# Optimization experiments

Hardware: AMD Instinct MI355X
Metric: run time of the kernel (lower is better)

## Reference

```python
import math
import jax, jax.numpy as jnp
import numpy as np

B, S, D = 4, 2048, 1024
H, HD = 16, 64
NUM_BUCKETS = 32
MAX_DISTANCE = 128
EPS = 1e-6
ENC_S = 512


def _relative_position_bucket(relative_position):
    # bidirectional=False path
    num_buckets = NUM_BUCKETS
    rp = -jnp.minimum(relative_position, 0)  # [S, S] nonneg
    max_exact = num_buckets // 2
    is_small = rp < max_exact
    scale = (num_buckets - max_exact) / math.log(MAX_DISTANCE / max_exact)
    large = max_exact + (jnp.log(jnp.maximum(rp, 1).astype(jnp.float32) / max_exact) * scale).astype(jnp.int32)
    large = jnp.minimum(large, num_buckets - 1)
    return jnp.where(is_small, rp, large)


def compute_bias(rel_emb, q_len, k_len):
    ctx = jnp.arange(q_len)[:, None]
    mem = jnp.arange(k_len)[None, :]
    bucket = _relative_position_bucket(mem - ctx)          # [q, k] int
    values = rel_emb[bucket]                                # [q, k, H]
    return jnp.transpose(values, (2, 0, 1))[None]           # [1, H, q, k]


def setup_inputs() -> dict:
    key = jax.random.key(0)
    ks = jax.random.split(key, 8)
    std = 0.02
    return {
        "input_ids": jax.random.normal(ks[0], (B, S, D), jnp.float32),
        "encoder_output": jax.random.normal(ks[1], (B, ENC_S, D), jnp.float32),
        "wq": jax.random.normal(ks[2], (D, H * HD), jnp.float32) * std,
        "wk": jax.random.normal(ks[3], (D, H * HD), jnp.float32) * std,
        "wv": jax.random.normal(ks[4], (D, H * HD), jnp.float32) * std,
        "wo": jax.random.normal(ks[5], (H * HD, D), jnp.float32) * std,
        "rel_emb": jax.random.normal(ks[6], (NUM_BUCKETS, H), jnp.float32) * std,
        "ln_w": jnp.ones((D,), jnp.float32),
    }


def reference(input_ids, encoder_output, wq, wk, wv, wo, rel_emb, ln_w):
    origin = input_ids
    # MT5LayerNorm: RMS norm, no mean subtraction, no bias
    variance = jnp.mean(jnp.square(input_ids.astype(jnp.float32)), axis=-1, keepdims=True)
    x = (input_ids * jax.lax.rsqrt(variance + EPS)) * ln_w

    q = (x @ wq).reshape(B, S, H, HD)
    k = (x @ wk).reshape(B, S, H, HD)
    v = (x @ wv).reshape(B, S, H, HD)

    # NOTE: T5-style attention has no 1/sqrt(d) scaling
    scores = jnp.einsum("bqhd,bkhd->bhqk", q, k)
    scores = scores + compute_bias(rel_emb, S, S)
    attn = jax.nn.softmax(scores, axis=-1)
    ctx = jnp.einsum("bhqk,bkhd->bqhd", attn, v).reshape(B, S, H * HD)
    attn_out = ctx @ wo

    # residual connection (dropout is identity at rate 0 / eval)
    return origin + attn_out
```

## Files before the change

### kernel.cpp

```cpp
#include <hip/hip_runtime.h>
#include <hip/hip_bf16.h>
#include <math.h>

#define S_LEN 2048
#define D_DIM 1024
#define NHEAD 16

typedef __attribute__((ext_vector_type(8))) short bf16x8;
typedef __attribute__((ext_vector_type(4))) float floatx4;

__device__ __forceinline__ short f32_bf16(float f) {
  union { float f; unsigned u; } v; v.f = f;
  unsigned r = v.u + 0x7FFFu + ((v.u >> 16) & 1u);
  return (short)(r >> 16);
}

__device__ __forceinline__ float exp2_fast(float x) {
#if __has_builtin(__builtin_amdgcn_exp2f)
  return __builtin_amdgcn_exp2f(x);
#else
  float r; asm("v_exp_f32 %0, %1" : "=v"(r) : "v"(x)); return r;
#endif
}

__device__ __forceinline__ void gload16(const void* g, void* l) {
  __builtin_amdgcn_global_load_lds((const __attribute__((address_space(1))) unsigned*)g,
                                   (__attribute__((address_space(3))) unsigned*)l,
                                   16, 0, 0);
}

__global__ __launch_bounds__(256) void prep_k(const float* __restrict__ x,
                                              const float* __restrict__ lnw,
                                              const float* __restrict__ wq,
                                              const float* __restrict__ wk,
                                              const float* __restrict__ wv,
                                              const float* __restrict__ wo,
                                              short* __restrict__ xb,
                                              short* __restrict__ oqkv,
                                              short* __restrict__ owo) {
  if (blockIdx.x < 8192) {
    int row = blockIdx.x;
    const float4* xr = (const float4*)(x + (size_t)row * D_DIM);
    float4 v = xr[threadIdx.x];
    float ss = v.x*v.x + v.y*v.y + v.z*v.z + v.w*v.w;
    #pragma unroll
    for (int off = 32; off > 0; off >>= 1) ss += __shfl_xor(ss, off);
    __shared__ float red[4];
    if ((threadIdx.x & 63) == 0) red[threadIdx.x >> 6] = ss;
    __syncthreads();
    float scale = rsqrtf((red[0]+red[1]+red[2]+red[3]) * (1.f/D_DIM) + 1e-6f);
    float4 wv4 = ((const float4*)lnw)[threadIdx.x];
    short4 o;
    o.x = f32_bf16(v.x*scale*wv4.x);
    o.y = f32_bf16(v.y*scale*wv4.y);
    o.z = f32_bf16(v.z*scale*wv4.z);
    o.w = f32_bf16(v.w*scale*wv4.w);
    ((short4*)xb)[(size_t)row*256 + threadIdx.x] = o;
  } else {
    __shared__ float tile[64][65];
    int id = blockIdx.x - 8192;
    int m  = id >> 8;
    int tt = id & 255;
    int tn = tt >> 4, tk = tt & 15;
    const float* src = (m == 0) ? wq : (m == 1) ? wk : (m == 2) ? wv : wo;
    float scale = (m == 0) ? 1.44269504f : 1.0f;
    int t = threadIdx.x;
    int kl  = t >> 4;
    int nl4 = t & 15;
    #pragma unroll
    for (int i = 0; i < 4; i++) {
      int k = i*16 + kl;
      float4 v = *(const float4*)&src[(size_t)(tk*64 + k)*1024 + tn*64 + nl4*4];
      tile[k][nl4*4+0] = v.x;
      tile[k][nl4*4+1] = v.y;
      tile[k][nl4*4+2] = v.z;
      tile[k][nl4*4+3] = v.w;
    }
    __syncthreads();
    short* dst = (m < 3) ? oqkv : owo;
    size_t nbase = (m < 3) ? (size_t)m * 1024 : 0;
    #pragma unroll
    for (int i = 0; i < 2; i++) {
      int idx = i*256 + t;
      int nl = idx >> 3;
      int g  = idx & 7;
      short tmp[8];
      #pragma unroll
      for (int j = 0; j < 8; j++) tmp[j] = f32_bf16(tile[g*8 + j][nl] * scale);
      *(bf16x8*)&dst[(nbase + tn*64 + nl)*1024 + tk*64 + g*8] = *(bf16x8*)tmp;
    }
  }
}

template<bool WRITE_VT, bool ADD_RES>
__global__ __launch_bounds__(512) void gemm256(const short* __restrict__ A,
                                               const short* __restrict__ Bt,
                                               short* __restrict__ Cb,
                                               float* __restrict__ Cf,
                                               const float* __restrict__ res,
                                               short* __restrict__ vt,
                                               int N, int NBN) {
  __shared__ __align__(16) short As[4][256*32];
  __shared__ __align__(16) short Bs[4][128*32];
  const int tid = threadIdx.x;
  const int w = tid >> 6, lane = tid & 63, quad = lane >> 4, l16 = lane & 15;
  const int wm = w >> 2, wn = w & 3;
  const int id = blockIdx.x;
  const int o = (id & 7) * (gridDim.x >> 3) + (id >> 3);
  const int bm = o / NBN, bn = o % NBN;
  const short* Ag = A  + (size_t)bm * 256 * 1024;
  const short* Bg = Bt + (size_t)bn * 128 * 1024;
  const int r4 = lane >> 2, c4 = lane & 3;
  const int lc  = c4 ^ ((r4 >> 1) & 3);
  const int swz = (quad ^ ((l16 >> 1) & 3)) * 8;

  floatx4 acc[8][2] = {};

  #define SA(t_) do {                                                          \
    gload16(Ag + (size_t)((w    )*16 + r4) * 1024 + (t_)*32 + lc*8,            \
            &As[(t_) & 3][(w    )*512]);                                       \
    gload16(Ag + (size_t)((w + 8)*16 + r4) * 1024 + (t_)*32 + lc*8,            \
            &As[(t_) & 3][(w + 8)*512]);                                       \
  } while (0)
  #define SB(t_) do {                                                          \
    gload16(Bg + (size_t)((w    )*16 + r4) * 1024 + (t_)*32 + lc*8,            \
            &Bs[(t_) & 3][(w    )*512]);                                       \
  } while (0)

  #define PH(t_, STG_, VMW_) do {                                              \
    const short* Ab = &As[(t_) & 3][0];                                        \
    const short* Bb = &Bs[(t_) & 3][0];                                        \
    bf16x8 af[8], bf0, bf1;                                                    \
    _Pragma("unroll")                                                          \
    for (int i = 0; i < 8; i++)                                                \
      af[i] = *(const bf16x8*)&Ab[(wm*128 + i*16 + l16)*32 + swz];             \
    bf0 = *(const bf16x8*)&Bb[(wn*32 +  0 + l16)*32 + swz];                    \
    if (STG_) SA((t_) + 3);                                                    \
    asm volatile("s_waitcnt lgkmcnt(0)");                                      \
    __builtin_amdgcn_sched_barrier(0);                                         \
    __builtin_amdgcn_s_setprio(1);                                             \
    _Pragma("unroll")                                                          \
    for (int i = 0; i < 8; i++)                                                \
      acc[i][0] = __builtin_amdgcn_mfma_f32_16x16x32_bf16(af[i], bf0, acc[i][0], 0, 0, 0); \
    __builtin_amdgcn_s_setprio(0);                                             \
    bf1 = *(const bf16x8*)&Bb[(wn*32 + 16 + l16)*32 + swz];                    \
    if (STG_) SB((t_) + 3);                                                    \
    asm volatile("s_waitcnt lgkmcnt(0)");                                      \
    __builtin_amdgcn_sched_barrier(0);                                         \
    __builtin_amdgcn_s_setprio(1);                                             \
    _Pragma("unroll")                                                          \
    for (int i = 0; i < 8; i++)                                                \
      acc[i][1] = __builtin_amdgcn_mfma_f32_16x16x32_bf16(af[i], bf1, acc[i][1], 0, 0, 0); \
    __builtin_amdgcn_s_setprio(0);                                             \
    asm volatile("s_waitcnt " VMW_);                                           \
    __builtin_amdgcn_s_barrier();                                              \
    __builtin_amdgcn_sched_barrier(0);                                         \
  } while (0)

  SA(0); SB(0); SA(1); SB(1); SA(2); SB(2);
  asm volatile("s_waitcnt vmcnt(6)");
  __builtin_amdgcn_s_barrier();
  __builtin_amdgcn_sched_barrier(0);

  #pragma unroll 1
  for (int t = 0; t < 29; ++t) PH(t, true, "vmcnt(6)");
  PH(29, false, "vmcnt(3)");
  PH(30, false, "vmcnt(0)");
  PH(31, false, "vmcnt(0)");
  #undef SA
  #undef SB
  #undef PH

  if (WRITE_VT && bn >= 16) {
    #pragma unroll
    for (int i = 0; i < 8; i++) {
      int row0 = bm*256 + wm*128 + i*16 + quad*4;
      int b = row0 >> 11, s = row0 & 2047;
      #pragma unroll
      for (int j = 0; j < 2; j++) {
        int hcol = (bn - 16)*128 + wn*32 + j*16 + l16;
        short4 st;
        st.x = f32_bf16(acc[i][j][0]);
        st.y = f32_bf16(acc[i][j][1]);
        st.z = f32_bf16(acc[i][j][2]);
        st.w = f32_bf16(acc[i][j][3]);
        int bh = (b << 4) + (hcol >> 6);
        *(short4*)&vt[((size_t)(bh*64 + (hcol & 63)))*2048 + s] = st;
      }
    }
    return;
  }

  #pragma unroll
  for (int i = 0; i < 8; i++) {
    int row0 = bm*256 + wm*128 + i*16 + quad*4;
    #pragma unroll
    for (int j = 0; j < 2; j++) {
      int col = bn*128 + wn*32 + j*16 + l16;
      #pragma unroll
      for (int r = 0; r < 4; r++) {
        size_t idx = (size_t)(row0 + r) * N + col;
        if (ADD_RES) Cf[idx] = res[idx] + acc[i][j][r];
        else         Cb[idx] = f32_bf16(acc[i][j][r]);
      }
    }
  }
}

__global__ __launch_bounds__(512) void flash_k(const short* __restrict__ qkv,
                                               const short* __restrict__ vt,
                                               const float* __restrict__ rel_emb,
                                               short* __restrict__ ctx) {
  __shared__ __align__(16) short Kb[2][64*64];
  __shared__ __align__(16) short Vb[2][64*64];
  __shared__ float lut2[132];

  const int L = blockIdx.x + 8*blockIdx.y;
  const int xcd = L & 7, kk_ = L >> 3;
  const int bh = xcd*8 + (kk_ >> 3);
  const int qt = kk_ & 7;
  const int b = bh >> 4, h = bh & 15;
  const int t = threadIdx.x, w = t >> 6, lane = t & 63, quad = lane >> 4, l16 = lane & 15;
  const float L2E = 1.44269504f;

  if (t < 129) {
    int rp = t, bucket;
    if (rp < 16) bucket = rp;
    else {
      bucket = 16 + (int)(logf((float)rp * 0.0625f) * (16.f / logf(8.f)));
      if (bucket > 31) bucket = 31;
    }
    lut2[t] = rel_emb[bucket*16 + h] * L2E;
  }
  const float bfut  = rel_emb[h] * L2E;
  const float bpast = rel_emb[31*16 + h] * L2E;
  const floatx4 bf4 = {bfut, bfut, bfut, bfut};
  const floatx4 bp4 = {bpast, bpast, bpast, bpast};
  const floatx4 zz4 = {0.f, 0.f, 0.f, 0.f};

  const int srow = lane >> 3;
  const int slc  = (lane & 7) ^ srow;
  const int rho  = w*8 + srow;
  const int kperm = 32*(rho >> 5) + 8*((rho >> 2) & 3) + 4*((rho >> 4) & 1) + (rho & 3);

  const short* kgU = qkv + ((size_t)b*S_LEN)*3072 + 1024 + h*64;
  const int    loK = kperm*3072 + slc*8;
  const short* vgU = vt + ((size_t)bh*64)*2048;
  const int    loV = rho*2048 + slc*8;

  bf16x8 qB[2][2];
  #pragma unroll
  for (int rb = 0; rb < 2; rb++) {
    const short* qb = qkv + ((size_t)(b*S_LEN + qt*256 + rb*128 + w*16 + l16))*3072 + h*64;
    qB[rb][0] = *(const bf16x8*)&qb[quad*8];
    qB[rb][1] = *(const bf16x8*)&qb[32 + quad*8];
  }

  floatx4 o[2][4] = {};
  floatx4 li4[2] = {};
  const short ONE = (short)0x3F80;
  bf16x8 onesA = {ONE, ONE, ONE, ONE, ONE, ONE, ONE, ONE};

  const int swz0 = (quad     ^ (l16 & 7)) * 8;
  const int swz1 = ((quad+4) ^ (l16 & 7)) * 8;

  #define STAGE(P_, KT_) do {                                                   \
    const short* ka_ = kgU + (size_t)(KT_)*196608 + loK;                        \
    gload16(ka_, &Kb[P_][(w*8)*64]);                                            \
    const short* va_ = vgU + loV + (KT_)*64;                                    \
    gload16(va_, &Vb[P_][(w*8)*64]);                                            \
  } while (0)

  #define BODY(P_, KT_) do {                                                    \
    __syncthreads();                                                            \
    if ((KT_) < 31) STAGE((P_) ^ 1, (KT_) + 1);                                 \
    bool boundary = ((KT_) >= 4*qt - 2) && ((KT_) <= 4*qt + 3);                 \
    floatx4 cinit = boundary ? zz4 : (((KT_) >= 4*qt) ? bf4 : bp4);             \
    floatx4 sc[2][4];                                                           \
    _Pragma("unroll")                                                           \
    for (int c = 0; c < 4; c++) {                                               \
      int rowA = (c*16 + l16)*64;                                               \
      bf16x8 ka0 = *(const bf16x8*)&Kb[P_][rowA + swz0];                        \
      bf16x8 ka1 = *(const bf16x8*)&Kb[P_][rowA + swz1];                        \
      _Pragma("unroll")                                                         \
      for (int rb = 0; rb < 2; rb++) {                                          \
        floatx4 z = __builtin_amdgcn_mfma_f32_16x16x32_bf16(ka0, qB[rb][0], cinit, 0, 0, 0); \
        z = __builtin_amdgcn_mfma_f32_16x16x32_bf16(ka1, qB[rb][1], z, 0, 0, 0);\
        sc[rb][c] = z;                                                          \
      }                                                                         \
    }                                                                           \
    if (boundary) {                                                             \
      _Pragma("unroll")                                                         \
      for (int rb = 0; rb < 2; rb++) {                                          \
        int q0 = qt*256 + rb*128 + w*16 + l16;                                  \
        _Pragma("unroll")                                                       \
        for (int c = 0; c < 4; c++) {                                           \
          int kk = (KT_)*64 + 32*(c >> 1) + 8*quad + 4*(c & 1);                 \
          _Pragma("unroll")                                                     \
          for (int r = 0; r < 4; r++) {                                         \
            int d = q0 - (kk + r);                                              \
            d = d < 0 ? 0 : (d > 128 ? 128 : d);                                \
            sc[rb][c][r] += lut2[d];                                            \
          }                                                                     \
        }                                                                       \
      }                                                                         \
    }                                                                           \
    _Pragma("unroll")                                                           \
    for (int rb = 0; rb < 2; rb++)                                              \
      _Pragma("unroll")                                                         \
      for (int c = 0; c < 4; c++)                                               \
        _Pragma("unroll")                                                       \
        for (int r = 0; r < 4; r++)                                             \
          sc[rb][c][r] = exp2_fast(sc[rb][c][r]);                               \
    bf16x8 pf[2][2];                                                            \
    _Pragma("unroll")                                                           \
    for (int rb = 0; rb < 2; rb++) {                                            \
      _Pragma("unroll")                                                         \
      for (int hh = 0; hh < 2; hh++) {                                          \
        union { bf16x8 v; unsigned u[4]; } pk;                                  \
        floatx4 a = sc[rb][2*hh], bb = sc[rb][2*hh + 1];                        \
        pk.u[0] = __builtin_amdgcn_perm(__float_as_uint(a[1]),  __float_as_uint(a[0]),  0x07060302); \
        pk.u[1] = __builtin_amdgcn_perm(__float_as_uint(a[3]),  __float_as_uint(a[2]),  0x07060302); \
        pk.u[2] = __builtin_amdgcn_perm(__float_as_uint(bb[1]), __float_as_uint(bb[0]), 0x07060302); \
        pk.u[3] = __builtin_amdgcn_perm(__float_as_uint(bb[3]), __float_as_uint(bb[2]), 0x07060302); \
        pf[rb][hh] = pk.v;                                                      \
      }                                                                         \
    }                                                                           \
    _Pragma("unroll")                                                           \
    for (int rb = 0; rb < 2; rb++) {                                            \
      li4[rb] = __builtin_amdgcn_mfma_f32_16x16x32_bf16(onesA, pf[rb][0], li4[rb], 0, 0, 0); \
      li4[rb] = __builtin_amdgcn_mfma_f32_16x16x32_bf16(onesA, pf[rb][1], li4[rb], 0, 0, 0); \
    }                                                                           \
    _Pragma("unroll")                                                           \
    for (int jj = 0; jj < 4; jj++) {                                            \
      int rowV = (jj*16 + l16)*64;                                              \
      bf16x8 va0 = *(const bf16x8*)&Vb[P_][rowV + swz0];                        \
      bf16x8 va1 = *(const bf16x8*)&Vb[P_][rowV + swz1];                        \
      _Pragma("unroll")                                                         \
      for (int rb = 0; rb < 2; rb++) {                                          \
        o[rb][jj] = __builtin_amdgcn_mfma_f32_16x16x32_bf16(va0, pf[rb][0], o[rb][jj], 0, 0, 0); \
        o[rb][jj] = __builtin_amdgcn_mfma_f32_16x16x32_bf16(va1, pf[rb][1], o[rb][jj], 0, 0, 0); \
      }                                                                         \
    }                                                                           \
  } while (0)

  STAGE(0, 0);
  for (int kt = 0; kt < 32; kt += 2) {
    BODY(0, kt);
    BODY(1, kt + 1);
  }

  #pragma unroll
  for (int rb = 0; rb < 2; rb++) {
    float inv = 1.f / li4[rb][0];
    size_t row = (size_t)(b*S_LEN + qt*256 + rb*128 + w*16 + l16);
    #pragma unroll
    for (int jj = 0; jj < 4; jj++) {
      short4 st;
      st.x = f32_bf16(o[rb][jj][0] * inv);
      st.y = f32_bf16(o[rb][jj][1] * inv);
      st.z = f32_bf16(o[rb][jj][2] * inv);
      st.w = f32_bf16(o[rb][jj][3] * inv);
      *(short4*)&ctx[row*1024 + h*64 + jj*16 + quad*4] = st;
    }
  }
  #undef STAGE
  #undef BODY
}

extern "C" void kernel_launch(void* const* d_in, const int* in_sizes, int n_in,
                              void* d_out, int out_size, void* d_ws, size_t ws_size,
                              hipStream_t stream) {
  const float* input_ids = (const float*)d_in[0];
  const float* wq      = (const float*)d_in[2];
  const float* wk      = (const float*)d_in[3];
  const float* wv      = (const float*)d_in[4];
  const float* wo      = (const float*)d_in[5];
  const float* rel_emb = (const float*)d_in[6];
  const float* ln_w    = (const float*)d_in[7];
  float* out = (float*)d_out;

  char* ws = (char*)d_ws;
  short* xb     = (short*)ws;  ws += (size_t)8192*1024*2;
  short* wqkv_t = (short*)ws;  ws += (size_t)3072*1024*2;
  short* wo_t   = (short*)ws;  ws += (size_t)1024*1024*2;
  short* qkv    = (short*)ws;  ws += (size_t)8192*3072*2;
  short* vt     = (short*)ws;  ws += (size_t)64*64*2048*2;
  short* ctx    = (short*)ws;  ws += (size_t)8192*1024*2;

  prep_k<<<8192 + 1024, 256, 0, stream>>>(input_ids, ln_w, wq, wk, wv, wo,
                                          xb, wqkv_t, wo_t);
  gemm256<true, false><<<768, 512, 0, stream>>>(xb, wqkv_t, qkv, nullptr,
                                                nullptr, vt, 3072, 24);
  flash_k<<<dim3(8, 64), 512, 0, stream>>>(qkv, vt, rel_emb, ctx);
  gemm256<false, true><<<256, 512, 0, stream>>>(ctx, wo_t, nullptr, out,
                                                input_ids, nullptr, 1024, 8);
}
```

Baseline: 269.1 us.

## Halve flash attention waves per block and give each wave more query rows

The attention kernel now runs 4 waves per block instead of 8, and each wave handles four 16-row query blocks instead of two. K fragments are read from shared memory once per tile and reused across all four row blocks, as are V fragments, which halves LDS reads per MFMA. The score/exp/pack work is also interleaved per row block, and each thread issues two K and two V async loads per stage. The cost is higher register pressure from twice the accumulators and fewer resident waves to hide latency.

```diff
diff --git a/kernel.cpp b/kernel.cpp
--- a/kernel.cpp
+++ b/kernel.cpp
@@ -207,7 +207,7 @@
   }
 }
 
-__global__ __launch_bounds__(512) void flash_k(const short* __restrict__ qkv,
+__global__ __launch_bounds__(256) void flash_k(const short* __restrict__ qkv,
                                                const short* __restrict__ vt,
                                                const float* __restrict__ rel_emb,
                                                short* __restrict__ ctx) {
@@ -240,24 +240,28 @@
 
   const int srow = lane >> 3;
   const int slc  = (lane & 7) ^ srow;
-  const int rho  = w*8 + srow;
-  const int kperm = 32*(rho >> 5) + 8*((rho >> 2) & 3) + 4*((rho >> 4) & 1) + (rho & 3);
+  const int rho0 = w*8 + srow;
+  const int rho1 = rho0 + 32;
+  const int kperm0 = 32*(rho0 >> 5) + 8*((rho0 >> 2) & 3) + 4*((rho0 >> 4) & 1) + (rho0 & 3);
+  const int kperm1 = 32*(rho1 >> 5) + 8*((rho1 >> 2) & 3) + 4*((rho1 >> 4) & 1) + (rho1 & 3);
 
   const short* kgU = qkv + ((size_t)b*S_LEN)*3072 + 1024 + h*64;
-  const int    loK = kperm*3072 + slc*8;
+  const int    loK0 = kperm0*3072 + slc*8;
+  const int    loK1 = kperm1*3072 + slc*8;
   const short* vgU = vt + ((size_t)bh*64)*2048;
-  const int    loV = rho*2048 + slc*8;
-
-  bf16x8 qB[2][2];
+  const int    loV0 = rho0*2048 + slc*8;
+  const int    loV1 = rho1*2048 + slc*8;
+
+  bf16x8 qB[4][2];
   #pragma unroll
-  for (int rb = 0; rb < 2; rb++) {
-    const short* qb = qkv + ((size_t)(b*S_LEN + qt*256 + rb*128 + w*16 + l16))*3072 + h*64;
+  for (int rb = 0; rb < 4; rb++) {
+    const short* qb = qkv + ((size_t)(b*S_LEN + qt*256 + rb*64 + w*16 + l16))*3072 + h*64;
     qB[rb][0] = *(const bf16x8*)&qb[quad*8];
     qB[rb][1] = *(const bf16x8*)&qb[32 + quad*8];
   }
 
-  floatx4 o[2][4] = {};
-  floatx4 li4[2] = {};
+  floatx4 o[4][4] = {};
+  floatx4 li4[4] = {};
   const short ONE = (short)0x3F80;
   bf16x8 onesA = {ONE, ONE, ONE, ONE, ONE, ONE, ONE, ONE};
 
@@ -265,10 +269,12 @@
   const int swz1 = ((quad+4) ^ (l16 & 7)) * 8;
 
   #define STAGE(P_, KT_) do {                                                   \
-    const short* ka_ = kgU + (size_t)(KT_)*196608 + loK;                        \
-    gload16(ka_, &Kb[P_][(w*8)*64]);                                            \
-    const short* va_ = vgU + loV + (KT_)*64;                                    \
-    gload16(va_, &Vb[P_][(w*8)*64]);                                            \
+    const short* ka_ = kgU + (size_t)(KT_)*196608;                              \
+    gload16(ka_ + loK0, &Kb[P_][(w*8)*64]);                                     \
+    gload16(ka_ + loK1, &Kb[P_][(w*8 + 32)*64]);                                \
+    const short* va_ = vgU + (size_t)(KT_)*64;                                  \
+    gload16(va_ + loV0, &Vb[P_][(w*8)*64]);                                     \
+    gload16(va_ + loV1, &Vb[P_][(w*8 + 32)*64]);                                \
   } while (0)
 
   #define BODY(P_, KT_) do {                                                    \
@@ -276,23 +282,25 @@
     if ((KT_) < 31) STAGE((P_) ^ 1, (KT_) + 1);                                 \
     bool boundary = ((KT_) >= 4*qt - 2) && ((KT_) <= 4*qt + 3);                 \
     floatx4 cinit = boundary ? zz4 : (((KT_) >= 4*qt) ? bf4 : bp4);             \
-    floatx4 sc[2][4];                                                           \
+    bf16x8 ka[4][2];                                                            \
     _Pragma("unroll")                                                           \
     for (int c = 0; c < 4; c++) {                                               \
       int rowA = (c*16 + l16)*64;                                               \
-      bf16x8 ka0 = *(const bf16x8*)&Kb[P_][rowA + swz0];                        \
-      bf16x8 ka1 = *(const bf16x8*)&Kb[P_][rowA + swz1];                        \
+      ka[c][0] = *(const bf16x8*)&Kb[P_][rowA + swz0];                          \
+      ka[c][1] = *(const bf16x8*)&Kb[P_][rowA + swz1];                          \
+    }                                                                           \
+    bf16x8 pf[4][2];                                                            \
+    _Pragma("unroll")                                                           \
+    for (int rb = 0; rb < 4; rb++) {                                            \
+      floatx4 sc[4];                                                            \
       _Pragma("unroll")                                                         \
-      for (int rb = 0; rb < 2; rb++) {                                          \
-        floatx4 z = __builtin_amdgcn_mfma_f32_16x16x32_bf16(ka0, qB[rb][0], cinit, 0, 0, 0); \
-        z = __builtin_amdgcn_mfma_f32_16x16x32_bf16(ka1, qB[rb][1], z, 0, 0, 0);\
-        sc[rb][c] = z;                                                          \
+      for (int c = 0; c < 4; c++) {                                             \
+        floatx4 z = __builtin_amdgcn_mfma_f32_16x16x32_bf16(ka[c][0], qB[rb][0], cinit, 0, 0, 0); \
+        z = __builtin_amdgcn_mfma_f32_16x16x32_bf16(ka[c][1], qB[rb][1], z, 0, 0, 0); \
+        sc[c] = z;                                                              \
       }                                                                         \
-    }                                                                           \
-    if (boundary) {                                                             \
-      _Pragma("unroll")                                                         \
-      for (int rb = 0; rb < 2; rb++) {                                          \
-        int q0 = qt*256 + rb*128 + w*16 + l16;                                  \
+      if (boundary) {                                                           \
+        int q0 = qt*256 + rb*64 + w*16 + l16;                                   \
         _Pragma("unroll")                                                       \
         for (int c = 0; c < 4; c++) {                                           \
           int kk = (KT_)*64 + 32*(c >> 1) + 8*quad + 4*(c & 1);                 \
@@ -300,25 +308,19 @@
           for (int r = 0; r < 4; r++) {                                         \
             int d = q0 - (kk + r);                                              \
             d = d < 0 ? 0 : (d > 128 ? 128 : d);                                \
-            sc[rb][c][r] += lut2[d];                                            \
+            sc[c][r] += lut2[d];                                                \
           }                                                                     \
         }                                                                       \
       }                                                                         \
-    }                                                                           \
-    _Pragma("unroll")                                                           \
-    for (int rb = 0; rb < 2; rb++)                                              \
       _Pragma("unroll")                                                         \
       for (int c = 0; c < 4; c++)                                               \
         _Pragma("unroll")                                                       \
         for (int r = 0; r < 4; r++)                                             \
-          sc[rb][c][r] = exp2_fast(sc[rb][c][r]);                               \
-    bf16x8 pf[2][2];                                                            \
-    _Pragma("unroll")                                                           \
-    for (int rb = 0; rb < 2; rb++) {                                            \
+          sc[c][r] = exp2_fast(sc[c][r]);                                       \
       _Pragma("unroll")                                                         \
       for (int hh = 0; hh < 2; hh++) {                                          \
         union { bf16x8 v; unsigned u[4]; } pk;                                  \
-        floatx4 a = sc[rb][2*hh], bb = sc[rb][2*hh + 1];                        \
+        floatx4 a = sc[2*hh], bb = sc[2*hh + 1];                                \
         pk.u[0] = __builtin_amdgcn_perm(__float_as_uint(a[1]),  __float_as_uint(a[0]),  0x07060302); \
         pk.u[1] = __builtin_amdgcn_perm(__float_as_uint(a[3]),  __float_as_uint(a[2]),  0x07060302); \
         pk.u[2] = __builtin_amdgcn_perm(__float_as_uint(bb[1]), __float_as_uint(bb[0]), 0x07060302); \
@@ -327,7 +329,7 @@
       }                                                                         \
     }                                                                           \
     _Pragma("unroll")                                                           \
-    for (int rb = 0; rb < 2; rb++) {                                            \
+    for (int rb = 0; rb < 4; rb++) {                                            \
       li4[rb] = __builtin_amdgcn_mfma_f32_16x16x32_bf16(onesA, pf[rb][0], li4[rb], 0, 0, 0); \
       li4[rb] = __builtin_amdgcn_mfma_f32_16x16x32_bf16(onesA, pf[rb][1], li4[rb], 0, 0, 0); \
     }                                                                           \
@@ -337,7 +339,7 @@
       bf16x8 va0 = *(const bf16x8*)&Vb[P_][rowV + swz0];                        \
       bf16x8 va1 = *(const bf16x8*)&Vb[P_][rowV + swz1];                        \
       _Pragma("unroll")                                                         \
-      for (int rb = 0; rb < 2; rb++) {                                          \
+      for (int rb = 0; rb < 4; rb++) {                                          \
         o[rb][jj] = __builtin_amdgcn_mfma_f32_16x16x32_bf16(va0, pf[rb][0], o[rb][jj], 0, 0, 0); \
         o[rb][jj] = __builtin_amdgcn_mfma_f32_16x16x32_bf16(va1, pf[rb][1], o[rb][jj], 0, 0, 0); \
       }                                                                         \
@@ -351,9 +353,9 @@
   }
 
   #pragma unroll
-  for (int rb = 0; rb < 2; rb++) {
+  for (int rb = 0; rb < 4; rb++) {
     float inv = 1.f / li4[rb][0];
-    size_t row = (size_t)(b*S_LEN + qt*256 + rb*128 + w*16 + l16);
+    size_t row = (size_t)(b*S_LEN + qt*256 + rb*64 + w*16 + l16);
     #pragma unroll
     for (int jj = 0; jj < 4; jj++) {
       short4 st;
@@ -392,7 +394,7 @@
                                           xb, wqkv_t, wo_t);
   gemm256<true, false><<<768, 512, 0, stream>>>(xb, wqkv_t, qkv, nullptr,
                                                 nullptr, vt, 3072, 24);
-  flash_k<<<dim3(8, 64), 512, 0, stream>>>(qkv, vt, rel_emb, ctx);
+  flash_k<<<dim3(8, 64), 256, 0, stream>>>(qkv, vt, rel_emb, ctx);
   gemm256<false, true><<<256, 512, 0, stream>>>(ctx, wo_t, nullptr, out,
                                                 input_ids, nullptr, 1024, 8);
 }
```

Result: slower. 319.3 us (+18.7%).
